# Kernel tuning notes

Hardware: AMD Instinct MI355X
Metric: run time of the kernel (lower is better)

Reference implementation:

```python
import jax, jax.numpy as jnp
import numpy as np

EMBED_DIM = 1024
NUM_HEADS = 16
HEAD_DIM = EMBED_DIM // NUM_HEADS


def setup_inputs() -> dict:
    key = jax.random.key(0)
    k_x, k_wqkv, k_bqkv, k_wo, k_bo = jax.random.split(key, 5)
    B, T, C = 8, 1024, EMBED_DIM
    s = 1.0 / np.sqrt(C)
    return {
        "x": jax.random.normal(k_x, (B, T, C), dtype=jnp.float32),
        "W_qkv": jax.random.uniform(k_wqkv, (C, 3 * C), minval=-s, maxval=s, dtype=jnp.float32),
        "b_qkv": jax.random.uniform(k_bqkv, (3 * C,), minval=-s, maxval=s, dtype=jnp.float32),
        "W_out": jax.random.uniform(k_wo, (C, C), minval=-s, maxval=s, dtype=jnp.float32),
        "b_out": jax.random.uniform(k_bo, (C,), minval=-s, maxval=s, dtype=jnp.float32),
    }


def reference(x, W_qkv, b_qkv, W_out, b_out):
    B, T, C = x.shape
    H, D = NUM_HEADS, HEAD_DIM
    qkv = x @ W_qkv + b_qkv                      # [B,T,3C]
    q, k, v = jnp.split(qkv, 3, axis=-1)
    q = q.reshape(B, T, H, D).transpose(0, 2, 1, 3)  # [B,H,T,D]
    k = k.reshape(B, T, H, D).transpose(0, 2, 1, 3)
    v = v.reshape(B, T, H, D).transpose(0, 2, 1, 3)
    scores = jnp.einsum("bhqd,bhkd->bhqk", q, k) / np.sqrt(D).astype(np.float32)
    causal = jnp.tril(jnp.ones((T, T), dtype=bool))
    scores = jnp.where(causal[None, None], scores, -jnp.inf)
    attn = jax.nn.softmax(scores, axis=-1)       # dropout is identity in eval
    out = jnp.einsum("bhqk,bhkd->bhqd", attn, v)
    out = out.transpose(0, 2, 1, 3).reshape(B, T, C)
    return out @ W_out + b_out
```

## Files before the change

### kernel.cpp

```cpp
#include <hip/hip_runtime.h>
#include <hip/hip_bf16.h>
#include <cstdint>

using bf16 = __hip_bfloat16;
typedef short short8 __attribute__((ext_vector_type(8)));
typedef float floatx4 __attribute__((ext_vector_type(4)));

#define QSCALE 0.1803368801111601f

__device__ __forceinline__ void async_load16(const bf16* g, bf16* l) {
    __builtin_amdgcn_global_load_lds(
        (const __attribute__((address_space(1))) uint32_t*)g,
        (__attribute__((address_space(3))) uint32_t*)l, 16, 0, 0);
}

__device__ __forceinline__ void bar_lgkm0() {
    asm volatile("s_waitcnt lgkmcnt(0)\ns_barrier" ::: "memory");
}
__device__ __forceinline__ void bar_vm4() {
    asm volatile("s_waitcnt vmcnt(4)\ns_barrier" ::: "memory");
}
__device__ __forceinline__ void bar_vm0() {
    asm volatile("s_waitcnt vmcnt(0)\ns_barrier" ::: "memory");
}
__device__ __forceinline__ void bar_vm4_lgkm0() {
    asm volatile("s_waitcnt vmcnt(4) lgkmcnt(0)\ns_barrier" ::: "memory");
}
__device__ __forceinline__ void bar_vm0_lgkm0() {
    asm volatile("s_waitcnt vmcnt(0) lgkmcnt(0)\ns_barrier" ::: "memory");
}

__device__ __forceinline__ uint32_t pack2(float a, float b) {
    union { bf16 h[2]; uint32_t u; } p;
    p.h[0] = __float2bfloat16(a);
    p.h[1] = __float2bfloat16(b);
    return p.u;
}

__global__ __launch_bounds__(256)
void cvt_bf16_kernel(const float* __restrict__ in, bf16* __restrict__ out) {
    const int i = (blockIdx.x * 256 + threadIdx.x) * 4;
    const float4 v = *(const float4*)(in + i);
    bf16 o[4] = {__float2bfloat16(v.x), __float2bfloat16(v.y),
                 __float2bfloat16(v.z), __float2bfloat16(v.w)};
    *(ushort4*)(out + i) = *(ushort4*)o;
}

__global__ __launch_bounds__(256)
void transpose_cvt_kernel(const float* __restrict__ in, bf16* __restrict__ out,
                          int R, int C) {
    __shared__ float tile[32][33];
    const int tx = threadIdx.x & 31, ty = threadIdx.x >> 5;
    const int c0 = blockIdx.x * 32, r0 = blockIdx.y * 32;
    #pragma unroll
    for (int i = 0; i < 32; i += 8)
        tile[ty + i][tx] = in[(size_t)(r0 + ty + i) * C + c0 + tx];
    __syncthreads();
    #pragma unroll
    for (int i = 0; i < 32; i += 8)
        out[(size_t)(c0 + ty + i) * R + r0 + tx] = __float2bfloat16(tile[tx][ty + i]);
}

template <int MODE>
__global__ __launch_bounds__(256, 3)
void gemm_bt_kernel(const bf16* __restrict__ A, const bf16* __restrict__ Bt,
                    const float* __restrict__ bias, int K,
                    bf16* __restrict__ q_ws, bf16* __restrict__ k_ws,
                    bf16* __restrict__ vt_ws, float* __restrict__ out, int N) {
    __shared__ bf16 As[3][128 * 32];
    __shared__ bf16 Bs[3][128 * 32];
    const int tid = threadIdx.x;
    const int wave = tid >> 6, lane = tid & 63;
    const int ln = lane & 15, quad = lane >> 4;
    const int wm = wave & 1, wn = wave >> 1;
    const int m0 = blockIdx.y * 128, n0 = blockIdx.x * 128;

    floatx4 acc[4][4] = {};
    const int nkt = K >> 5;

    #pragma unroll
    for (int t = 0; t < 2; ++t) {
        const int k0 = t << 5;
        #pragma unroll
        for (int c = 0; c < 2; ++c) {
            const int e = (c * 256 + tid) * 8;
            async_load16(A + (size_t)(m0 + (e >> 5)) * K + k0 + (e & 31),
                         &As[t][(c * 256 + wave * 64) * 8]);
        }
        #pragma unroll
        for (int c = 0; c < 2; ++c) {
            const int e = (c * 256 + tid) * 8;
            async_load16(Bt + (size_t)(n0 + (e >> 5)) * K + k0 + (e & 31),
                         &Bs[t][(c * 256 + wave * 64) * 8]);
        }
    }

    for (int kt = 0; kt < nkt; ++kt) {
        const int cur = kt % 3;
        if (kt + 1 < nkt) bar_vm4_lgkm0();
        else              bar_vm0_lgkm0();

        if (kt + 2 < nkt) {
            const int nxt = (kt + 2) % 3;
            const int k0 = (kt + 2) << 5;
            #pragma unroll
            for (int c = 0; c < 2; ++c) {
                const int e = (c * 256 + tid) * 8;
                async_load16(A + (size_t)(m0 + (e >> 5)) * K + k0 + (e & 31),
                             &As[nxt][(c * 256 + wave * 64) * 8]);
            }
            #pragma unroll
            for (int c = 0; c < 2; ++c) {
                const int e = (c * 256 + tid) * 8;
                async_load16(Bt + (size_t)(n0 + (e >> 5)) * K + k0 + (e & 31),
                             &Bs[nxt][(c * 256 + wave * 64) * 8]);
            }
        }

        short8 af[4], bfr[4];
        #pragma unroll
        for (int i = 0; i < 4; ++i) {
            af[i]  = *(const short8*)&As[cur][(wm * 64 + i * 16 + ln) * 32 + quad * 8];
            bfr[i] = *(const short8*)&Bs[cur][(wn * 64 + i * 16 + ln) * 32 + quad * 8];
        }
        #pragma unroll
        for (int mi = 0; mi < 4; ++mi)
            #pragma unroll
            for (int ni = 0; ni < 4; ++ni)
                acc[mi][ni] = __builtin_amdgcn_mfma_f32_16x16x32_bf16(
                    af[mi], bfr[ni], acc[mi][ni], 0, 0, 0);
    }

    #pragma unroll
    for (int ni = 0; ni < 4; ++ni) {
        const int col = n0 + wn * 64 + ni * 16 + ln;
        const float bv = bias[col];
        if (MODE == 0) {
            const int which = col >> 10;
            const int cc = col & 1023;
            const int h = cc >> 6, d = cc & 63;
            #pragma unroll
            for (int mi = 0; mi < 4; ++mi) {
                const int rowb = m0 + wm * 64 + mi * 16 + quad * 4;
                if (which == 2) {
                    const int bb = rowb >> 10, t = rowb & 1023;
                    const int tl = t & 63;
                    const int tt = (t & ~63) + ((((tl >> 3) ^ (d & 7)) << 3) | (tl & 7));
                    uint2 w2 = { pack2(acc[mi][ni][0] + bv, acc[mi][ni][1] + bv),
                                 pack2(acc[mi][ni][2] + bv, acc[mi][ni][3] + bv) };
                    *(uint2*)&vt_ws[((size_t)(bb * 16 + h) * 64 + d) * 1024 + tt] = w2;
                } else {
                    bf16* dst = (which == 0) ? q_ws : k_ws;
                    #pragma unroll
                    for (int r = 0; r < 4; ++r) {
                        const int row = rowb + r;
                        const int bb = row >> 10, t = row & 1023;
                        float v = acc[mi][ni][r] + bv;
                        if (which == 0) v *= QSCALE;
                        const int dd = (((d >> 3) ^ (t & 7)) << 3) | (d & 7);
                        dst[((size_t)(bb * 16 + h) * 1024 + t) * 64 + dd] =
                            __float2bfloat16(v);
                    }
                }
            }
        } else {
            #pragma unroll
            for (int mi = 0; mi < 4; ++mi) {
                const int rowb = m0 + wm * 64 + mi * 16 + quad * 4;
                #pragma unroll
                for (int r = 0; r < 4; ++r)
                    out[(size_t)(rowb + r) * N + col] = acc[mi][ni][r] + bv;
            }
        }
    }
}

__global__ __launch_bounds__(256, 4)
void attn_kernel(const bf16* __restrict__ Q, const bf16* __restrict__ K,
                 const bf16* __restrict__ Vt, bf16* __restrict__ O) {
    constexpr int T = 1024;
    __shared__ bf16 QPs[64 * 64];
    __shared__ bf16 Ks[2][64 * 64];
    __shared__ bf16 Vts[2][64 * 64];

    const int bh = blockIdx.y;
    const int tid = threadIdx.x;
    const int wave = tid >> 6, lane = tid & 63;
    const int ln = lane & 15, quad = lane >> 4;

    const bf16* Kg = K + (size_t)bh * T * 64;
    const bf16* Vg = Vt + (size_t)bh * 64 * T;
    const int b = bh >> 4, h = bh & 15;

    #pragma unroll
    for (int phase = 0; phase < 2; ++phase) {
        const int jt = phase ? 15 - blockIdx.x : blockIdx.x;
        const int q0 = jt * 64;
        const int nkt = jt + 1;

        bar_lgkm0();

        const bf16* Qg = Q + (size_t)bh * T * 64 + (size_t)q0 * 64;
        #pragma unroll
        for (int c = 0; c < 2; ++c)
            async_load16(Qg + (size_t)(c * 256 + tid) * 8,
                         &QPs[(c * 256 + wave * 64) * 8]);
        #pragma unroll
        for (int c = 0; c < 2; ++c)
            async_load16(Kg + (size_t)(c * 256 + tid) * 8,
                         &Ks[0][(c * 256 + wave * 64) * 8]);
        #pragma unroll
        for (int c = 0; c < 2; ++c) {
            const int e = (c * 256 + tid) * 8;
            async_load16(Vg + (size_t)(e >> 6) * T + (e & 63),
                         &Vts[0][(c * 256 + wave * 64) * 8]);
        }
        bar_vm0();

        short8 bq[2];
        #pragma unroll
        for (int ks = 0; ks < 2; ++ks) {
            const int row = wave * 16 + ln;
            const int ch = (ks * 4 + quad) ^ (row & 7);
            bq[ks] = *(const short8*)&QPs[row * 64 + ch * 8];
        }

        floatx4 oacc[4] = {};
        float rl = 0.f;
        const int qbw = q0 + wave * 16;

        for (int kt = 0; kt < nkt; ++kt) {
            const int cur = kt & 1;
            bar_lgkm0();
            if (kt + 1 < nkt) {
                const int nxt = cur ^ 1;
                #pragma unroll
                for (int c = 0; c < 2; ++c)
                    async_load16(Kg + (size_t)(kt + 1) * 4096 + (size_t)(c * 256 + tid) * 8,
                                 &Ks[nxt][(c * 256 + wave * 64) * 8]);
                #pragma unroll
                for (int c = 0; c < 2; ++c) {
                    const int e = (c * 256 + tid) * 8;
                    async_load16(Vg + (size_t)(e >> 6) * T + (kt + 1) * 64 + (e & 63),
                                 &Vts[nxt][(c * 256 + wave * 64) * 8]);
                }
                bar_vm4();
            } else {
                bar_vm0();
            }

            const int k0 = kt * 64;
            if (k0 > qbw + 15) continue;
            const bool tail = (k0 + 63 > qbw);

            floatx4 sacc[4] = {};
            #pragma unroll
            for (int nj = 0; nj < 4; ++nj) {
                if (tail && k0 + nj * 16 > qbw + 15) continue;
                #pragma unroll
                for (int ks = 0; ks < 2; ++ks) {
                    const int row = nj * 16 + ln;
                    const int ch = (ks * 4 + quad) ^ (row & 7);
                    const short8 ak = *(const short8*)&Ks[cur][row * 64 + ch * 8];
                    sacc[nj] = __builtin_amdgcn_mfma_f32_16x16x32_bf16(
                        ak, bq[ks], sacc[nj], 0, 0, 0);
                }
            }

            if (tail) {
                const int qq = qbw + ln;
                #pragma unroll
                for (int nj = 0; nj < 4; ++nj)
                    #pragma unroll
                    for (int r = 0; r < 4; ++r) {
                        const int kk = k0 + nj * 16 + quad * 4 + r;
                        if (kk > qq) sacc[nj][r] = -1e30f;
                    }
            }

            {
                float rs = 0.f;
                const int qrow = wave * 16 + ln;
                #pragma unroll
                for (int nj = 0; nj < 4; ++nj) {
                    float p[4];
                    #pragma unroll
                    for (int r = 0; r < 4; ++r) {
                        p[r] = exp2f(sacc[nj][r]);
                        rs += p[r];
                    }
                    const int kcol = nj * 16 + quad * 4;
                    const int ch = (kcol >> 3) ^ (qrow & 7);
                    uint2 w2 = { pack2(p[0], p[1]), pack2(p[2], p[3]) };
                    *(uint2*)&QPs[qrow * 64 + ch * 8 + (kcol & 7)] = w2;
                }
                rl += rs;
            }

            #pragma unroll
            for (int ks4 = 0; ks4 < 2; ++ks4) {
                const int qrow = wave * 16 + ln;
                const int chp = (ks4 * 4 + quad) ^ (qrow & 7);
                const short8 bp = *(const short8*)&QPs[qrow * 64 + chp * 8];
                #pragma unroll
                for (int dt = 0; dt < 4; ++dt) {
                    const int row = dt * 16 + ln;
                    const int ch = (ks4 * 4 + quad) ^ (row & 7);
                    const short8 av = *(const short8*)&Vts[cur][row * 64 + ch * 8];
                    oacc[dt] = __builtin_amdgcn_mfma_f32_16x16x32_bf16(
                        av, bp, oacc[dt], 0, 0, 0);
                }
            }
        }

        {
            float l = rl;
            l += __shfl_xor(l, 16, 64);
            l += __shfl_xor(l, 32, 64);
            const float inv = 1.0f / l;
            const int t = q0 + wave * 16 + ln;
            const size_t rowb = ((size_t)b * 1024 + t) * 1024 + h * 64;
            #pragma unroll
            for (int dt = 0; dt < 4; ++dt) {
                uint2 w2 = { pack2(oacc[dt][0] * inv, oacc[dt][1] * inv),
                             pack2(oacc[dt][2] * inv, oacc[dt][3] * inv) };
                *(uint2*)&O[rowb + dt * 16 + quad * 4] = w2;
            }
        }
    }
}

extern "C" void kernel_launch(void* const* d_in, const int* in_sizes, int n_in,
                              void* d_out, int out_size, void* d_ws, size_t ws_size,
                              hipStream_t stream) {
    const float* x     = (const float*)d_in[0];
    const float* W_qkv = (const float*)d_in[1];
    const float* b_qkv = (const float*)d_in[2];
    const float* W_out = (const float*)d_in[3];
    const float* b_out = (const float*)d_in[4];
    float* out = (float*)d_out;

    char* ws = (char*)d_ws;
    const size_t MB = 1u << 20;
    bf16* x_bf   = (bf16*)(ws + 0);
    bf16* wqkv_t = (bf16*)(ws + 16 * MB);
    bf16* wout_t = (bf16*)(ws + 22 * MB);
    bf16* q_ws   = (bf16*)(ws + 24 * MB);
    bf16* k_ws   = (bf16*)(ws + 40 * MB);
    bf16* vt_ws  = (bf16*)(ws + 56 * MB);
    bf16* ao_ws  = (bf16*)(ws + 72 * MB);

    cvt_bf16_kernel<<<8192, 256, 0, stream>>>(x, x_bf);
    transpose_cvt_kernel<<<dim3(96, 32), 256, 0, stream>>>(W_qkv, wqkv_t, 1024, 3072);
    transpose_cvt_kernel<<<dim3(32, 32), 256, 0, stream>>>(W_out, wout_t, 1024, 1024);

    gemm_bt_kernel<0><<<dim3(24, 64), 256, 0, stream>>>(
        x_bf, wqkv_t, b_qkv, 1024, q_ws, k_ws, vt_ws, nullptr, 3072);

    attn_kernel<<<dim3(8, 128), 256, 0, stream>>>(q_ws, k_ws, vt_ws, ao_ws);

    gemm_bt_kernel<1><<<dim3(8, 64), 256, 0, stream>>>(
        ao_ws, wout_t, b_out, 1024, nullptr, nullptr, nullptr, out, 1024);
}
```

Measured before the change: 251.2 us.

## Double-buffer GEMM with XOR-swizzled LDS, raise occupancy, merge weight transposes

```diff
diff --git a/kernel.cpp b/kernel.cpp
--- a/kernel.cpp
+++ b/kernel.cpp
@@ -22,9 +22,6 @@
 }
 __device__ __forceinline__ void bar_vm0() {
     asm volatile("s_waitcnt vmcnt(0)\ns_barrier" ::: "memory");
-}
-__device__ __forceinline__ void bar_vm4_lgkm0() {
-    asm volatile("s_waitcnt vmcnt(4) lgkmcnt(0)\ns_barrier" ::: "memory");
 }
 __device__ __forceinline__ void bar_vm0_lgkm0() {
     asm volatile("s_waitcnt vmcnt(0) lgkmcnt(0)\ns_barrier" ::: "memory");
@@ -47,11 +44,17 @@
 }
 
 __global__ __launch_bounds__(256)
-void transpose_cvt_kernel(const float* __restrict__ in, bf16* __restrict__ out,
-                          int R, int C) {
+void transpose_cvt2_kernel(const float* __restrict__ inA, bf16* __restrict__ outA,
+                           const float* __restrict__ inB, bf16* __restrict__ outB) {
     __shared__ float tile[32][33];
     const int tx = threadIdx.x & 31, ty = threadIdx.x >> 5;
-    const int c0 = blockIdx.x * 32, r0 = blockIdx.y * 32;
+    const bool isB = blockIdx.x >= 96;
+    const float* __restrict__ in = isB ? inB : inA;
+    bf16* __restrict__ out = isB ? outB : outA;
+    const int C = isB ? 1024 : 3072;
+    const int bx = isB ? blockIdx.x - 96 : blockIdx.x;
+    const int c0 = bx * 32, r0 = blockIdx.y * 32;
+    const int R = 1024;
     #pragma unroll
     for (int i = 0; i < 32; i += 8)
         tile[ty + i][tx] = in[(size_t)(r0 + ty + i) * C + c0 + tx];
@@ -62,13 +65,13 @@
 }
 
 template <int MODE>
-__global__ __launch_bounds__(256, 3)
+__global__ __launch_bounds__(256, 5)
 void gemm_bt_kernel(const bf16* __restrict__ A, const bf16* __restrict__ Bt,
                     const float* __restrict__ bias, int K,
                     bf16* __restrict__ q_ws, bf16* __restrict__ k_ws,
                     bf16* __restrict__ vt_ws, float* __restrict__ out, int N) {
-    __shared__ bf16 As[3][128 * 32];
-    __shared__ bf16 Bs[3][128 * 32];
+    __shared__ bf16 As[2][128 * 32];
+    __shared__ bf16 Bs[2][128 * 32];
     const int tid = threadIdx.x;
     const int wave = tid >> 6, lane = tid & 63;
     const int ln = lane & 15, quad = lane >> 4;
@@ -79,49 +82,52 @@
     const int nkt = K >> 5;
 
     #pragma unroll
-    for (int t = 0; t < 2; ++t) {
-        const int k0 = t << 5;
-        #pragma unroll
-        for (int c = 0; c < 2; ++c) {
-            const int e = (c * 256 + tid) * 8;
-            async_load16(A + (size_t)(m0 + (e >> 5)) * K + k0 + (e & 31),
-                         &As[t][(c * 256 + wave * 64) * 8]);
-        }
-        #pragma unroll
-        for (int c = 0; c < 2; ++c) {
-            const int e = (c * 256 + tid) * 8;
-            async_load16(Bt + (size_t)(n0 + (e >> 5)) * K + k0 + (e & 31),
-                         &Bs[t][(c * 256 + wave * 64) * 8]);
-        }
+    for (int c = 0; c < 2; ++c) {
+        const int e = (c * 256 + tid) * 8;
+        const int row = e >> 5;
+        const int gch = ((((e >> 3) & 3) ^ ((row >> 1) & 3)) << 3);
+        async_load16(A + (size_t)(m0 + row) * K + gch,
+                     &As[0][(c * 256 + wave * 64) * 8]);
+    }
+    #pragma unroll
+    for (int c = 0; c < 2; ++c) {
+        const int e = (c * 256 + tid) * 8;
+        const int row = e >> 5;
+        const int gch = ((((e >> 3) & 3) ^ ((row >> 1) & 3)) << 3);
+        async_load16(Bt + (size_t)(n0 + row) * K + gch,
+                     &Bs[0][(c * 256 + wave * 64) * 8]);
     }
 
     for (int kt = 0; kt < nkt; ++kt) {
-        const int cur = kt % 3;
-        if (kt + 1 < nkt) bar_vm4_lgkm0();
-        else              bar_vm0_lgkm0();
-
-        if (kt + 2 < nkt) {
-            const int nxt = (kt + 2) % 3;
-            const int k0 = (kt + 2) << 5;
+        const int cur = kt & 1;
+        bar_vm0_lgkm0();
+
+        if (kt + 1 < nkt) {
+            const int k0 = (kt + 1) << 5;
             #pragma unroll
             for (int c = 0; c < 2; ++c) {
                 const int e = (c * 256 + tid) * 8;
-                async_load16(A + (size_t)(m0 + (e >> 5)) * K + k0 + (e & 31),
-                             &As[nxt][(c * 256 + wave * 64) * 8]);
+                const int row = e >> 5;
+                const int gch = ((((e >> 3) & 3) ^ ((row >> 1) & 3)) << 3);
+                async_load16(A + (size_t)(m0 + row) * K + k0 + gch,
+                             &As[cur ^ 1][(c * 256 + wave * 64) * 8]);
             }
             #pragma unroll
             for (int c = 0; c < 2; ++c) {
                 const int e = (c * 256 + tid) * 8;
-                async_load16(Bt + (size_t)(n0 + (e >> 5)) * K + k0 + (e & 31),
-                             &Bs[nxt][(c * 256 + wave * 64) * 8]);
-            }
-        }
-
+                const int row = e >> 5;
+                const int gch = ((((e >> 3) & 3) ^ ((row >> 1) & 3)) << 3);
+                async_load16(Bt + (size_t)(n0 + row) * K + k0 + gch,
+                             &Bs[cur ^ 1][(c * 256 + wave * 64) * 8]);
+            }
+        }
+
+        const int chq = ((quad ^ ((ln >> 1) & 3)) << 3);
         short8 af[4], bfr[4];
         #pragma unroll
         for (int i = 0; i < 4; ++i) {
-            af[i]  = *(const short8*)&As[cur][(wm * 64 + i * 16 + ln) * 32 + quad * 8];
-            bfr[i] = *(const short8*)&Bs[cur][(wn * 64 + i * 16 + ln) * 32 + quad * 8];
+            af[i]  = *(const short8*)&As[cur][(wm * 64 + i * 16 + ln) * 32 + chq];
+            bfr[i] = *(const short8*)&Bs[cur][(wn * 64 + i * 16 + ln) * 32 + chq];
         }
         #pragma unroll
         for (int mi = 0; mi < 4; ++mi)
@@ -351,8 +357,7 @@
     bf16* ao_ws  = (bf16*)(ws + 72 * MB);
 
     cvt_bf16_kernel<<<8192, 256, 0, stream>>>(x, x_bf);
-    transpose_cvt_kernel<<<dim3(96, 32), 256, 0, stream>>>(W_qkv, wqkv_t, 1024, 3072);
-    transpose_cvt_kernel<<<dim3(32, 32), 256, 0, stream>>>(W_out, wout_t, 1024, 1024);
+    transpose_cvt2_kernel<<<dim3(128, 32), 256, 0, stream>>>(W_qkv, wqkv_t, W_out, wout_t);
 
     gemm_bt_kernel<0><<<dim3(24, 64), 256, 0, stream>>>(
         x_bf, wqkv_t, b_qkv, 1024, q_ws, k_ws, vt_ws, nullptr, 3072);
```

After: 280.7 us. +11.8%, slower.
